# Kernel optimization log

Hardware: AMD Instinct MI355X
Metric: run time of the kernel (lower is better)

The kernel has to match this reference:

```python
import jax, jax.numpy as jnp
import numpy as np

N = 131072          # collocation points per dataset
C_WAVE = 1.0        # wave speed c
DIMS = [2, 256, 256, 256, 256, 1]


def _glorot(k, shape):
    fan_in, fan_out = shape
    std = jnp.sqrt(2.0 / (fan_in + fan_out)).astype(jnp.float32)
    return std * jax.random.normal(k, shape, dtype=jnp.float32)


def setup_inputs() -> dict:
    key = jax.random.key(0)
    ks = jax.random.split(key, 16)
    inp = {}
    for i in range(5):
        inp[f"W{i}"] = _glorot(ks[i], (DIMS[i], DIMS[i + 1]))
        inp[f"b{i}"] = jnp.zeros((DIMS[i + 1],), jnp.float32)
    inp["tx_equation"] = jax.random.uniform(ks[10], (N, 2), dtype=jnp.float32)
    inp["tx_init"] = jax.random.uniform(ks[11], (N, 2), dtype=jnp.float32)
    # initial condition points have t=0 in practice; values don't affect the math pattern
    inp["tx_init"] = inp["tx_init"].at[:, 0].set(0.0)
    inp["tx_bound"] = jax.random.uniform(ks[12], (N, 2), dtype=jnp.float32)
    return inp


def _mlp(params, tx):
    # tanh MLP: (..., 2) -> (..., 1)
    h = tx
    for W, b in params[:-1]:
        h = jnp.tanh(h @ W + b)
    W, b = params[-1]
    return h @ W + b


def reference(W0, b0, W1, b1, W2, b2, W3, b3, W4, b4,
              tx_equation, tx_init, tx_bound):
    params = [(W0, b0), (W1, b1), (W2, b2), (W3, b3), (W4, b4)]

    def u_scalar(tx):  # tx: (2,) -> scalar u(t, x)
        return _mlp(params, tx[None, :])[0, 0]

    # PDE residual: u_tt - c^2 * u_xx via per-point Hessian diagonal (input_diagonal_hessian)
    hess = jax.vmap(jax.hessian(u_scalar))(tx_equation)      # (N, 2, 2)
    u_tt = hess[:, 0, 0]
    u_xx = hess[:, 1, 1]
    pde_residual = (u_tt - (C_WAVE ** 2) * u_xx)[:, None]     # (N, 1)

    # Initial conditions: u and du/dt (input_gradient)
    u_init, g = jax.vmap(jax.value_and_grad(u_scalar))(tx_init)  # (N,), (N, 2)
    u_phi = u_init[:, None]                                   # (N, 1)
    du_dt_psi = g[:, 0][:, None]                              # (N, 1)

    # Boundary: plain forward
    u_bound = _mlp(params, tx_bound)                          # (N, 1)

    return jnp.stack([pde_residual, u_phi, du_dt_psi, u_bound], axis=0)  # (4, N, 1)
```

## Files before the change

### kernel.cpp

```cpp
#include <hip/hip_runtime.h>
#include <math.h>

#define N_PTS 131072
#define HID   256

typedef __attribute__((ext_vector_type(8)))  _Float16 f16x8;
typedef __attribute__((ext_vector_type(4)))  float    f32x4;
typedef __attribute__((ext_vector_type(16))) float    f32x16;
typedef unsigned int u32;
typedef __attribute__((address_space(1))) const u32 gu32;
typedef __attribute__((address_space(3))) u32       lu32;

#define LDS_ACT 0
#define LDS_B   32768
#define LDS_SZ  49152

__device__ __forceinline__ int act_addr(int row, int kbyte) {
    return row * 512 + ((kbyte + ((row & 31) << 4)) & 511);
}
__device__ __forceinline__ void tanh_f1(float z, float& h, float& f1) {
    float s = __expf(2.0f * z);
    float r = __builtin_amdgcn_rcpf(s + 1.0f);
    h  = fmaf(-2.0f, r, 1.0f);
    f1 = (1.0f - h) * (1.0f + h);
}

__global__ void prep_w(const float* __restrict__ W1, const float* __restrict__ W2,
                       const float* __restrict__ W3, char* __restrict__ ws)
{
    int idx = blockIdx.x * 256 + threadIdx.x;
    int l = idx >> 16;
    int e = idx & 65535;
    int k = e >> 8, n = e & 255;
    const float* W = (l == 0) ? W1 : (l == 1) ? W2 : W3;
    float w = W[e];
    int kc = k >> 4, hh = (k >> 3) & 1, kl = k & 7;
    int wq = n >> 6, j = (n >> 5) & 1, nn = n & 31;
    size_t base = (size_t)((l * 16 + kc) * 4 + wq) * 2048;
    int byte_in = hh * 1024 + j * 512 + nn * 16 + kl * 2;
    *(_Float16*)(ws + base + byte_in) = (_Float16)w;
}

template<int S, int PTS>
__global__ void __launch_bounds__(256, 3)
pinn_mfma(const float* __restrict__ W0, const float* __restrict__ b0,
          const float* __restrict__ b1, const float* __restrict__ b2,
          const float* __restrict__ b3,
          const float* __restrict__ W4, const float* __restrict__ b4,
          const char* __restrict__ wpre,
          const float* __restrict__ tx, float* __restrict__ out)
{
    extern __shared__ char lds[];
    const int tid  = threadIdx.x;
    const int lane = tid & 63;
    const int wid  = tid >> 6;
    const int l31  = lane & 31;
    const int hh   = lane >> 5;
    const int h16  = hh << 4;
    const int pbase = blockIdx.x * PTS;
    constexpr int CG = 256 / PTS;
    constexpr int NC = 256 / CG;
    const int ep  = tid / CG;
    const int ec0 = (tid % CG) * NC;

    {
        const float tt = tx[2 * (pbase + ep) + 0];
        const float xx = tx[2 * (pbase + ep) + 1];
        for (int cb = ec0; cb < ec0 + NC; cb += 8) {
            alignas(16) float w0r[8], w1r[8], bb[8];
            *(f32x4*)&w0r[0] = *(const f32x4*)(W0 + cb);
            *(f32x4*)&w0r[4] = *(const f32x4*)(W0 + cb + 4);
            *(f32x4*)&w1r[0] = *(const f32x4*)(W0 + HID + cb);
            *(f32x4*)&w1r[4] = *(const f32x4*)(W0 + HID + cb + 4);
            *(f32x4*)&bb[0]  = *(const f32x4*)(b0 + cb);
            *(f32x4*)&bb[4]  = *(const f32x4*)(b0 + cb + 4);
            f16x8 vhi[S];
            #pragma unroll
            for (int j = 0; j < 8; ++j) {
                float z = fmaf(tt, w0r[j], fmaf(xx, w1r[j], bb[j]));
                float h, f1;
                tanh_f1(z, h, f1);
                vhi[0][j] = (_Float16)h;
                if (S == 2) {
                    vhi[1][j] = (_Float16)(f1 * w0r[j]);
                } else if (S == 4) {
                    float d1 = w0r[j] + w1r[j];
                    float d2 = w0r[j] - w1r[j];
                    float f2 = -2.0f * h * f1;
                    vhi[1][j] = (_Float16)(f1 * d1);
                    vhi[2][j] = (_Float16)(f1 * d2);
                    vhi[3][j] = (_Float16)(f2 * d1 * d2);
                }
            }
            #pragma unroll
            for (int s2 = 0; s2 < S; ++s2) {
                int row = ep * S + s2;
                *(f16x8*)(lds + LDS_ACT + act_addr(row, cb * 2)) = vhi[s2];
            }
        }
    }

    const int c0 = wid * 64 + l31;
    const float b1a = b1[c0], b1b = b1[c0 + 32];
    const float b2a = b2[c0], b2b = b2[c0 + 32];
    const float b3a = b3[c0], b3b = b3[c0 + 32];

    const char* srcW = wpre + (size_t)wid * 2048 + lane * 16;
    char* dstW = lds + LDS_B + wid * 4096 + lane * 16;
    __builtin_amdgcn_sched_barrier(0);
    __builtin_amdgcn_global_load_lds((gu32*)srcW,          (lu32*)dstW,          16, 0, 0);
    __builtin_amdgcn_global_load_lds((gu32*)(srcW + 1024), (lu32*)(dstW + 1024), 16, 0, 0);
    asm volatile("s_waitcnt lgkmcnt(0)" ::: "memory");
    __builtin_amdgcn_sched_barrier(0);
    __builtin_amdgcn_s_barrier();
    __builtin_amdgcn_sched_barrier(0);

    for (int l = 0; l < 3; ++l) {
        const float biasA = (l == 0) ? b1a : (l == 1) ? b2a : b3a;
        const float biasB = (l == 0) ? b1b : (l == 1) ? b2b : b3b;
        const char* srcL = srcW + (size_t)l * 131072;

        f32x16 acc[2][2];
        #pragma unroll
        for (int i = 0; i < 2; ++i)
            #pragma unroll
            for (int j = 0; j < 2; ++j)
                acc[i][j] = (f32x16){0.f,0.f,0.f,0.f,0.f,0.f,0.f,0.f,
                                     0.f,0.f,0.f,0.f,0.f,0.f,0.f,0.f};

        #pragma unroll
        for (int ph = 0; ph < 16; ++ph) {
            asm volatile("s_waitcnt vmcnt(0)" ::: "memory");

            const char* bslab = lds + LDS_B + wid * 4096 + (ph & 1) * 2048 + hh * 1024;
            const int kbyte = ph * 32 + h16;
            f16x8 av[2], bv[2];
            #pragma unroll
            for (int i = 0; i < 2; ++i)
                av[i] = *(const f16x8*)(lds + LDS_ACT + act_addr(i * 32 + l31, kbyte));
            #pragma unroll
            for (int j = 0; j < 2; ++j)
                bv[j] = *(const f16x8*)(bslab + j * 512 + l31 * 16);

            if (ph < 15 || l < 2) {
                const char* s = srcL + (size_t)(ph + 1) * 8192;
                char* d = dstW + ((ph + 1) & 1) * 2048;
                __builtin_amdgcn_global_load_lds((gu32*)s,          (lu32*)d,          16, 0, 0);
                __builtin_amdgcn_global_load_lds((gu32*)(s + 1024), (lu32*)(d + 1024), 16, 0, 0);
            }

            __builtin_amdgcn_s_setprio(1);
            acc[0][0] = __builtin_amdgcn_mfma_f32_32x32x16_f16(av[0], bv[0], acc[0][0], 0, 0, 0);
            acc[0][1] = __builtin_amdgcn_mfma_f32_32x32x16_f16(av[0], bv[1], acc[0][1], 0, 0, 0);
            acc[1][0] = __builtin_amdgcn_mfma_f32_32x32x16_f16(av[1], bv[0], acc[1][0], 0, 0, 0);
            acc[1][1] = __builtin_amdgcn_mfma_f32_32x32x16_f16(av[1], bv[1], acc[1][1], 0, 0, 0);
            __builtin_amdgcn_s_setprio(0);
        }
        __builtin_amdgcn_s_barrier();

        const bool lastL = (l == 2);
        #pragma unroll
        for (int i = 0; i < 2; ++i) {
            #pragma unroll
            for (int j = 0; j < 2; ++j) {
                const int colj = wid * 64 + j * 32 + l31;
                const float bias = j ? biasB : biasA;
                const int rtb = i * 32 + 4 * hh;
                #pragma unroll
                for (int q = 0; q < 4; ++q) {
                    const int rb = rtb + 8 * q;
                    if (S == 4) {
                        float z0 = acc[i][j][4*q+0] + bias;
                        float z1 = acc[i][j][4*q+1];
                        float z2 = acc[i][j][4*q+2];
                        float zm = acc[i][j][4*q+3];
                        float h, f1;
                        tanh_f1(z0, h, f1);
                        float f2 = -2.0f * h * f1;
                        if (!lastL) {
                            *(_Float16*)(lds + LDS_ACT + act_addr(rb+0, colj*2)) = (_Float16)h;
                            *(_Float16*)(lds + LDS_ACT + act_addr(rb+1, colj*2)) = (_Float16)(f1 * z1);
                            *(_Float16*)(lds + LDS_ACT + act_addr(rb+2, colj*2)) = (_Float16)(f1 * z2);
                        }
                        *(_Float16*)(lds + LDS_ACT + act_addr(rb+3, colj*2)) =
                            (_Float16)(fmaf(f1, zm, f2 * z1 * z2));
                    } else if (S == 2) {
                        #pragma unroll
                        for (int pp = 0; pp < 2; ++pp) {
                            float z0 = acc[i][j][4*q+2*pp+0] + bias;
                            float zd = acc[i][j][4*q+2*pp+1];
                            float h, f1;
                            tanh_f1(z0, h, f1);
                            *(_Float16*)(lds + LDS_ACT + act_addr(rb+2*pp+0, colj*2)) = (_Float16)h;
                            *(_Float16*)(lds + LDS_ACT + act_addr(rb+2*pp+1, colj*2)) = (_Float16)(f1 * zd);
                        }
                    } else {
                        #pragma unroll
                        for (int m = 0; m < 4; ++m) {
                            float z0 = acc[i][j][4*q+m] + bias;
                            float h, f1;
                            tanh_f1(z0, h, f1);
                            *(_Float16*)(lds + LDS_ACT + act_addr(rb+m, colj*2)) = (_Float16)h;
                        }
                    }
                }
            }
        }
        asm volatile("s_waitcnt lgkmcnt(0)" ::: "memory");
        __builtin_amdgcn_sched_barrier(0);
        __builtin_amdgcn_s_barrier();
        __builtin_amdgcn_sched_barrier(0);
    }

    if (S == 4) {
        const int p   = tid >> 4;
        const int seg = tid & 15;
        const int k0  = seg * 16;
        const int row = 4 * p + 3;
        float d = 0.0f;
        #pragma unroll
        for (int kb = 0; kb < 16; kb += 8) {
            f16x8 h8 = *(const f16x8*)(lds + LDS_ACT + act_addr(row, (k0 + kb) * 2));
            alignas(16) float wv[8];
            *(f32x4*)&wv[0] = *(const f32x4*)(W4 + k0 + kb);
            *(f32x4*)&wv[4] = *(const f32x4*)(W4 + k0 + kb + 4);
            #pragma unroll
            for (int j = 0; j < 8; ++j) d = fmaf((float)h8[j], wv[j], d);
        }
        #pragma unroll
        for (int off = 8; off > 0; off >>= 1) d += __shfl_down(d, off, 16);
        if (seg == 0) out[0 * N_PTS + pbase + p] = d;
    } else {
        const int row = tid >> 2;
        const int seg = tid & 3;
        const int k0  = seg * 64;
        float d = 0.0f;
        #pragma unroll
        for (int kb = 0; kb < 64; kb += 8) {
            f16x8 h8 = *(const f16x8*)(lds + LDS_ACT + act_addr(row, (k0 + kb) * 2));
            alignas(16) float wv[8];
            *(f32x4*)&wv[0] = *(const f32x4*)(W4 + k0 + kb);
            *(f32x4*)&wv[4] = *(const f32x4*)(W4 + k0 + kb + 4);
            #pragma unroll
            for (int j = 0; j < 8; ++j) d = fmaf((float)h8[j], wv[j], d);
        }
        d += __shfl_down(d, 2, 4);
        d += __shfl_down(d, 1, 4);
        if (seg == 0) {
            if (S == 2) {
                const int p = row >> 1;
                if ((row & 1) == 0) out[1 * N_PTS + pbase + p] = d + b4[0];
                else                out[2 * N_PTS + pbase + p] = d;
            } else {
                out[3 * N_PTS + pbase + row] = d + b4[0];
            }
        }
    }
}

extern "C" void kernel_launch(void* const* d_in, const int* in_sizes, int n_in,
                              void* d_out, int out_size, void* d_ws, size_t ws_size,
                              hipStream_t stream) {
    const float* W0 = (const float*)d_in[0];
    const float* b0 = (const float*)d_in[1];
    const float* W1 = (const float*)d_in[2];
    const float* b1 = (const float*)d_in[3];
    const float* W2 = (const float*)d_in[4];
    const float* b2 = (const float*)d_in[5];
    const float* W3 = (const float*)d_in[6];
    const float* b3 = (const float*)d_in[7];
    const float* W4 = (const float*)d_in[8];
    const float* b4 = (const float*)d_in[9];
    const float* tx_eq    = (const float*)d_in[10];
    const float* tx_init  = (const float*)d_in[11];
    const float* tx_bound = (const float*)d_in[12];
    float* out = (float*)d_out;
    char* wpre = (char*)d_ws;

    prep_w<<<768, 256, 0, stream>>>(W1, W2, W3, wpre);
    pinn_mfma<4,16><<<N_PTS/16, 256, LDS_SZ, stream>>>(W0,b0,b1,b2,b3,W4,b4,wpre,tx_eq,   out);
    pinn_mfma<2,32><<<N_PTS/32, 256, LDS_SZ, stream>>>(W0,b0,b1,b2,b3,W4,b4,wpre,tx_init, out);
    pinn_mfma<1,64><<<N_PTS/64, 256, LDS_SZ, stream>>>(W0,b0,b1,b2,b3,W4,b4,wpre,tx_bound,out);
}
```

Before: 610.6 us.

## Split each block's output columns across eight waves instead of four

Measured after the change: 578.8 us. 1.05x faster.

```diff
diff --git a/kernel.cpp b/kernel.cpp
--- a/kernel.cpp
+++ b/kernel.cpp
@@ -35,14 +35,14 @@
     const float* W = (l == 0) ? W1 : (l == 1) ? W2 : W3;
     float w = W[e];
     int kc = k >> 4, hh = (k >> 3) & 1, kl = k & 7;
-    int wq = n >> 6, j = (n >> 5) & 1, nn = n & 31;
-    size_t base = (size_t)((l * 16 + kc) * 4 + wq) * 2048;
-    int byte_in = hh * 1024 + j * 512 + nn * 16 + kl * 2;
+    int wq = n >> 5, nn = n & 31;
+    size_t base = (size_t)((l * 16 + kc) * 8 + wq) * 1024;
+    int byte_in = hh * 512 + nn * 16 + kl * 2;
     *(_Float16*)(ws + base + byte_in) = (_Float16)w;
 }
 
 template<int S, int PTS>
-__global__ void __launch_bounds__(256, 3)
+__global__ void __launch_bounds__(512, 4)
 pinn_mfma(const float* __restrict__ W0, const float* __restrict__ b0,
           const float* __restrict__ b1, const float* __restrict__ b2,
           const float* __restrict__ b3,
@@ -58,7 +58,7 @@
     const int hh   = lane >> 5;
     const int h16  = hh << 4;
     const int pbase = blockIdx.x * PTS;
-    constexpr int CG = 256 / PTS;
+    constexpr int CG = 512 / PTS;
     constexpr int NC = 256 / CG;
     const int ep  = tid / CG;
     const int ec0 = (tid % CG) * NC;
@@ -100,108 +100,93 @@
         }
     }
 
-    const int c0 = wid * 64 + l31;
-    const float b1a = b1[c0], b1b = b1[c0 + 32];
-    const float b2a = b2[c0], b2b = b2[c0 + 32];
-    const float b3a = b3[c0], b3b = b3[c0 + 32];
-
-    const char* srcW = wpre + (size_t)wid * 2048 + lane * 16;
-    char* dstW = lds + LDS_B + wid * 4096 + lane * 16;
+    const int c0 = wid * 32 + l31;
+    const float b1a = b1[c0];
+    const float b2a = b2[c0];
+    const float b3a = b3[c0];
+
+    const char* srcW = wpre + (size_t)wid * 1024 + lane * 16;
+    char* dstW = lds + LDS_B + wid * 2048 + lane * 16;
+
     __builtin_amdgcn_sched_barrier(0);
-    __builtin_amdgcn_global_load_lds((gu32*)srcW,          (lu32*)dstW,          16, 0, 0);
-    __builtin_amdgcn_global_load_lds((gu32*)(srcW + 1024), (lu32*)(dstW + 1024), 16, 0, 0);
+    __builtin_amdgcn_global_load_lds((gu32*)srcW, (lu32*)dstW, 16, 0, 0);
     asm volatile("s_waitcnt lgkmcnt(0)" ::: "memory");
     __builtin_amdgcn_sched_barrier(0);
     __builtin_amdgcn_s_barrier();
     __builtin_amdgcn_sched_barrier(0);
 
     for (int l = 0; l < 3; ++l) {
-        const float biasA = (l == 0) ? b1a : (l == 1) ? b2a : b3a;
-        const float biasB = (l == 0) ? b1b : (l == 1) ? b2b : b3b;
+        const float bias = (l == 0) ? b1a : (l == 1) ? b2a : b3a;
         const char* srcL = srcW + (size_t)l * 131072;
 
-        f32x16 acc[2][2];
-        #pragma unroll
-        for (int i = 0; i < 2; ++i)
-            #pragma unroll
-            for (int j = 0; j < 2; ++j)
-                acc[i][j] = (f32x16){0.f,0.f,0.f,0.f,0.f,0.f,0.f,0.f,
-                                     0.f,0.f,0.f,0.f,0.f,0.f,0.f,0.f};
+        f32x16 acc0 = (f32x16){0.f,0.f,0.f,0.f,0.f,0.f,0.f,0.f,
+                               0.f,0.f,0.f,0.f,0.f,0.f,0.f,0.f};
+        f32x16 acc1 = acc0;
 
         #pragma unroll
         for (int ph = 0; ph < 16; ++ph) {
             asm volatile("s_waitcnt vmcnt(0)" ::: "memory");
 
-            const char* bslab = lds + LDS_B + wid * 4096 + (ph & 1) * 2048 + hh * 1024;
+            const char* bslab = lds + LDS_B + wid * 2048 + (ph & 1) * 1024 + hh * 512;
             const int kbyte = ph * 32 + h16;
-            f16x8 av[2], bv[2];
-            #pragma unroll
-            for (int i = 0; i < 2; ++i)
-                av[i] = *(const f16x8*)(lds + LDS_ACT + act_addr(i * 32 + l31, kbyte));
-            #pragma unroll
-            for (int j = 0; j < 2; ++j)
-                bv[j] = *(const f16x8*)(bslab + j * 512 + l31 * 16);
+            f16x8 av0 = *(const f16x8*)(lds + LDS_ACT + act_addr(l31,      kbyte));
+            f16x8 av1 = *(const f16x8*)(lds + LDS_ACT + act_addr(32 + l31, kbyte));
+            f16x8 bv  = *(const f16x8*)(bslab + l31 * 16);
 
             if (ph < 15 || l < 2) {
-                const char* s = srcL + (size_t)(ph + 1) * 8192;
-                char* d = dstW + ((ph + 1) & 1) * 2048;
-                __builtin_amdgcn_global_load_lds((gu32*)s,          (lu32*)d,          16, 0, 0);
-                __builtin_amdgcn_global_load_lds((gu32*)(s + 1024), (lu32*)(d + 1024), 16, 0, 0);
+                __builtin_amdgcn_global_load_lds(
+                    (gu32*)(srcL + (size_t)(ph + 1) * 8192),
+                    (lu32*)(dstW + ((ph + 1) & 1) * 1024), 16, 0, 0);
             }
 
             __builtin_amdgcn_s_setprio(1);
-            acc[0][0] = __builtin_amdgcn_mfma_f32_32x32x16_f16(av[0], bv[0], acc[0][0], 0, 0, 0);
-            acc[0][1] = __builtin_amdgcn_mfma_f32_32x32x16_f16(av[0], bv[1], acc[0][1], 0, 0, 0);
-            acc[1][0] = __builtin_amdgcn_mfma_f32_32x32x16_f16(av[1], bv[0], acc[1][0], 0, 0, 0);
-            acc[1][1] = __builtin_amdgcn_mfma_f32_32x32x16_f16(av[1], bv[1], acc[1][1], 0, 0, 0);
+            acc0 = __builtin_amdgcn_mfma_f32_32x32x16_f16(av0, bv, acc0, 0, 0, 0);
+            acc1 = __builtin_amdgcn_mfma_f32_32x32x16_f16(av1, bv, acc1, 0, 0, 0);
             __builtin_amdgcn_s_setprio(0);
         }
         __builtin_amdgcn_s_barrier();
 
         const bool lastL = (l == 2);
+        const int colj = wid * 32 + l31;
         #pragma unroll
         for (int i = 0; i < 2; ++i) {
-            #pragma unroll
-            for (int j = 0; j < 2; ++j) {
-                const int colj = wid * 64 + j * 32 + l31;
-                const float bias = j ? biasB : biasA;
-                const int rtb = i * 32 + 4 * hh;
-                #pragma unroll
-                for (int q = 0; q < 4; ++q) {
-                    const int rb = rtb + 8 * q;
-                    if (S == 4) {
-                        float z0 = acc[i][j][4*q+0] + bias;
-                        float z1 = acc[i][j][4*q+1];
-                        float z2 = acc[i][j][4*q+2];
-                        float zm = acc[i][j][4*q+3];
+            const f32x16& A = i ? acc1 : acc0;
+            const int rtb = i * 32 + 4 * hh;
+            #pragma unroll
+            for (int q = 0; q < 4; ++q) {
+                const int rb = rtb + 8 * q;
+                if (S == 4) {
+                    float z0 = A[4*q+0] + bias;
+                    float z1 = A[4*q+1];
+                    float z2 = A[4*q+2];
+                    float zm = A[4*q+3];
+                    float h, f1;
+                    tanh_f1(z0, h, f1);
+                    float f2 = -2.0f * h * f1;
+                    if (!lastL) {
+                        *(_Float16*)(lds + LDS_ACT + act_addr(rb+0, colj*2)) = (_Float16)h;
+                        *(_Float16*)(lds + LDS_ACT + act_addr(rb+1, colj*2)) = (_Float16)(f1 * z1);
+                        *(_Float16*)(lds + LDS_ACT + act_addr(rb+2, colj*2)) = (_Float16)(f1 * z2);
+                    }
+                    *(_Float16*)(lds + LDS_ACT + act_addr(rb+3, colj*2)) =
+                        (_Float16)(fmaf(f1, zm, f2 * z1 * z2));
+                } else if (S == 2) {
+                    #pragma unroll
+                    for (int pp = 0; pp < 2; ++pp) {
+                        float z0 = A[4*q+2*pp+0] + bias;
+                        float zd = A[4*q+2*pp+1];
                         float h, f1;
                         tanh_f1(z0, h, f1);
-                        float f2 = -2.0f * h * f1;
-                        if (!lastL) {
-                            *(_Float16*)(lds + LDS_ACT + act_addr(rb+0, colj*2)) = (_Float16)h;
-                            *(_Float16*)(lds + LDS_ACT + act_addr(rb+1, colj*2)) = (_Float16)(f1 * z1);
-                            *(_Float16*)(lds + LDS_ACT + act_addr(rb+2, colj*2)) = (_Float16)(f1 * z2);
-                        }
-                        *(_Float16*)(lds + LDS_ACT + act_addr(rb+3, colj*2)) =
-                            (_Float16)(fmaf(f1, zm, f2 * z1 * z2));
-                    } else if (S == 2) {
-                        #pragma unroll
-                        for (int pp = 0; pp < 2; ++pp) {
-                            float z0 = acc[i][j][4*q+2*pp+0] + bias;
-                            float zd = acc[i][j][4*q+2*pp+1];
-                            float h, f1;
-                            tanh_f1(z0, h, f1);
-                            *(_Float16*)(lds + LDS_ACT + act_addr(rb+2*pp+0, colj*2)) = (_Float16)h;
-                            *(_Float16*)(lds + LDS_ACT + act_addr(rb+2*pp+1, colj*2)) = (_Float16)(f1 * zd);
-                        }
-                    } else {
-                        #pragma unroll
-                        for (int m = 0; m < 4; ++m) {
-                            float z0 = acc[i][j][4*q+m] + bias;
-                            float h, f1;
-                            tanh_f1(z0, h, f1);
-                            *(_Float16*)(lds + LDS_ACT + act_addr(rb+m, colj*2)) = (_Float16)h;
-                        }
+                        *(_Float16*)(lds + LDS_ACT + act_addr(rb+2*pp+0, colj*2)) = (_Float16)h;
+                        *(_Float16*)(lds + LDS_ACT + act_addr(rb+2*pp+1, colj*2)) = (_Float16)(f1 * zd);
+                    }
+                } else {
+                    #pragma unroll
+                    for (int m = 0; m < 4; ++m) {
+                        float z0 = A[4*q+m] + bias;
+                        float h, f1;
+                        tanh_f1(z0, h, f1);
+                        *(_Float16*)(lds + LDS_ACT + act_addr(rb+m, colj*2)) = (_Float16)h;
                     }
                 }
             }
@@ -213,13 +198,27 @@
     }
 
     if (S == 4) {
-        const int p   = tid >> 4;
-        const int seg = tid & 15;
-        const int k0  = seg * 16;
+        const int p   = tid >> 5;
+        const int seg = tid & 31;
+        const int k0  = seg * 8;
         const int row = 4 * p + 3;
+        f16x8 h8 = *(const f16x8*)(lds + LDS_ACT + act_addr(row, k0 * 2));
+        alignas(16) float wv[8];
+        *(f32x4*)&wv[0] = *(const f32x4*)(W4 + k0);
+        *(f32x4*)&wv[4] = *(const f32x4*)(W4 + k0 + 4);
         float d = 0.0f;
         #pragma unroll
-        for (int kb = 0; kb < 16; kb += 8) {
+        for (int j = 0; j < 8; ++j) d = fmaf((float)h8[j], wv[j], d);
+        #pragma unroll
+        for (int off = 16; off > 0; off >>= 1) d += __shfl_down(d, off, 32);
+        if (seg == 0) out[0 * N_PTS + pbase + p] = d;
+    } else {
+        const int row = tid >> 3;
+        const int seg = tid & 7;
+        const int k0  = seg * 32;
+        float d = 0.0f;
+        #pragma unroll
+        for (int kb = 0; kb < 32; kb += 8) {
             f16x8 h8 = *(const f16x8*)(lds + LDS_ACT + act_addr(row, (k0 + kb) * 2));
             alignas(16) float wv[8];
             *(f32x4*)&wv[0] = *(const f32x4*)(W4 + k0 + kb);
@@ -227,25 +226,9 @@
             #pragma unroll
             for (int j = 0; j < 8; ++j) d = fmaf((float)h8[j], wv[j], d);
         }
-        #pragma unroll
-        for (int off = 8; off > 0; off >>= 1) d += __shfl_down(d, off, 16);
-        if (seg == 0) out[0 * N_PTS + pbase + p] = d;
-    } else {
-        const int row = tid >> 2;
-        const int seg = tid & 3;
-        const int k0  = seg * 64;
-        float d = 0.0f;
-        #pragma unroll
-        for (int kb = 0; kb < 64; kb += 8) {
-            f16x8 h8 = *(const f16x8*)(lds + LDS_ACT + act_addr(row, (k0 + kb) * 2));
-            alignas(16) float wv[8];
-            *(f32x4*)&wv[0] = *(const f32x4*)(W4 + k0 + kb);
-            *(f32x4*)&wv[4] = *(const f32x4*)(W4 + k0 + kb + 4);
-            #pragma unroll
-            for (int j = 0; j < 8; ++j) d = fmaf((float)h8[j], wv[j], d);
-        }
-        d += __shfl_down(d, 2, 4);
-        d += __shfl_down(d, 1, 4);
+        d += __shfl_down(d, 4, 8);
+        d += __shfl_down(d, 2, 8);
+        d += __shfl_down(d, 1, 8);
         if (seg == 0) {
             if (S == 2) {
                 const int p = row >> 1;
@@ -278,7 +261,7 @@
     char* wpre = (char*)d_ws;
 
     prep_w<<<768, 256, 0, stream>>>(W1, W2, W3, wpre);
-    pinn_mfma<4,16><<<N_PTS/16, 256, LDS_SZ, stream>>>(W0,b0,b1,b2,b3,W4,b4,wpre,tx_eq,   out);
-    pinn_mfma<2,32><<<N_PTS/32, 256, LDS_SZ, stream>>>(W0,b0,b1,b2,b3,W4,b4,wpre,tx_init, out);
-    pinn_mfma<1,64><<<N_PTS/64, 256, LDS_SZ, stream>>>(W0,b0,b1,b2,b3,W4,b4,wpre,tx_bound,out);
-}
+    pinn_mfma<4,16><<<N_PTS/16, 512, LDS_SZ, stream>>>(W0,b0,b1,b2,b3,W4,b4,wpre,tx_eq,   out);
+    pinn_mfma<2,32><<<N_PTS/32, 512, LDS_SZ, stream>>>(W0,b0,b1,b2,b3,W4,b4,wpre,tx_init, out);
+    pinn_mfma<1,64><<<N_PTS/64, 512, LDS_SZ, stream>>>(W0,b0,b1,b2,b3,W4,b4,wpre,tx_bound,out);
+}
```
